# Performance work log

Measured on AMD Instinct MI355X. Metric: run time of the kernel, lower is better.

## Reference

```python
import jax, jax.numpy as jnp
import numpy as np

V, E, H = 32000, 128, 128

def setup_inputs() -> dict:
    key = jax.random.key(0)
    ks = jax.random.split(key, 12)
    s = 0.05
    x = jax.random.randint(ks[0], (256, 512), 0, V)
    emb = jax.random.normal(ks[1], (V, E), jnp.float32) * s
    Wi = jax.random.normal(ks[2], (E + H, H), jnp.float32) * s
    bi = jnp.zeros((H,), jnp.float32)
    Wf = jax.random.normal(ks[3], (E + H, H), jnp.float32) * s
    bf = jnp.zeros((H,), jnp.float32)
    Wc = jax.random.normal(ks[4], (E + H, H), jnp.float32) * s
    bc = jnp.zeros((H,), jnp.float32)
    Wo = jax.random.normal(ks[5], (E + H, H), jnp.float32) * s
    bo = jnp.zeros((H,), jnp.float32)
    Wout = jax.random.normal(ks[6], (H, V), jnp.float32) * s
    bout = jnp.zeros((V,), jnp.float32)
    return {"x": x, "emb": emb, "Wi": Wi, "bi": bi, "Wf": Wf, "bf": bf,
            "Wc": Wc, "bc": bc, "Wo": Wo, "bo": bo, "Wout": Wout, "bout": bout}

def reference(x, emb, Wi, bi, Wf, bf, Wc, bc, Wo, bo, Wout, bout):
    B, T = x.shape
    xe = emb[x]                       # [B, T, E] embedding gather
    xe_t = jnp.swapaxes(xe, 0, 1)     # [T, B, E] for scan over time

    def step(carry, e_t):
        h, c = carry
        comb = jnp.concatenate([e_t, h], axis=1)          # [B, E+H]
        f = jax.nn.sigmoid(comb @ Wf + bf)
        i = jax.nn.sigmoid(comb @ Wi + bi)
        o = jax.nn.sigmoid(comb @ Wo + bo)
        c_ = jnp.tanh(comb @ Wc + bc)
        c = f * c + i * c_
        h = o * jnp.tanh(c)
        return (h, c), None

    h0 = jnp.zeros((B, H), xe.dtype)
    c0 = jnp.zeros((B, H), xe.dtype)
    (h, _), _ = jax.lax.scan(step, (h0, c0), xe_t)
    return h @ Wout + bout            # [B, V] logits from final hidden state
```

## Files before the change

kernel.cpp:

```cpp
#include <hip/hip_runtime.h>

constexpr int TT = 512;
constexpr int BB = 256;
constexpr int HH = 128;
constexpr int VV = 32000;

typedef _Float16 h2 __attribute__((ext_vector_type(2)));
typedef _Float16 f16x4 __attribute__((ext_vector_type(4)));
typedef _Float16 f16x8 __attribute__((ext_vector_type(8)));
typedef float f32x4 __attribute__((ext_vector_type(4)));

struct __align__(16) H2x4 { h2 a, b, c, d; };

__device__ __forceinline__ h2 pkrtz(float a, float b) {
  return __builtin_bit_cast(h2, __builtin_amdgcn_cvt_pkrtz(a, b));
}
__device__ __forceinline__ float fexp2(float x) {
  return __builtin_amdgcn_exp2f(x);
}
__device__ __forceinline__ float frcp(float x) {
  return __builtin_amdgcn_rcpf(x);
}
template <int CTRL>
__device__ __forceinline__ float qmov(float v) {
  return __builtin_bit_cast(
      float, __builtin_amdgcn_mov_dpp(__builtin_bit_cast(int, v), CTRL, 0xf,
                                      0xf, true));
}

constexpr float SC_SIG = -1.4426950408889634f;
constexpr float SC_TANH = 2.8853900817779268f;

__global__ __launch_bounds__(256, 4) void wprep(
    const float* __restrict__ Wi, const float* __restrict__ bi,
    const float* __restrict__ Wf, const float* __restrict__ bf,
    const float* __restrict__ Wc, const float* __restrict__ bc,
    const float* __restrict__ Wo, const float* __restrict__ bo,
    _Float16* __restrict__ Wct, float* __restrict__ bcat) {
  const int n = blockIdx.x;
  const int g = n & 3;
  const int u = n >> 2;
  const float* Wg = (g == 0) ? Wi : (g == 1) ? Wf : (g == 2) ? Wc : Wo;
  const float* bg = (g == 0) ? bi : (g == 1) ? bf : (g == 2) ? bc : bo;
  const float sc = (g == 2) ? SC_TANH : SC_SIG;
  const int k = threadIdx.x;
  Wct[(size_t)n * 256 + k] = (_Float16)(Wg[(size_t)k * HH + u] * sc);
  if (k == 0) bcat[n] = bg[u] * sc;
}

__global__ __launch_bounds__(512, 2) void lstm_rec(
    const int* __restrict__ x, const float* __restrict__ emb,
    const _Float16* __restrict__ Wct, const float* __restrict__ bcat,
    _Float16* __restrict__ hbf) {
  const int b = blockIdx.x;
  const int tid = threadIdx.x;
  const int w = tid >> 6;
  const int l = tid & 63;
  const int n16 = l & 15;
  const int quad = l >> 4;
  const int g = n16 & 3;
  const int nts = n16 >> 2;
  const int u = 16 * w + 4 * nts + quad;
  const int xcol = 4 * u + g;

  __shared__ int xrow[TT];
  __shared__ __align__(16) _Float16 comb[2][HH];
  __shared__ __align__(16) _Float16 xch[64][516];

  xrow[tid] = x[(size_t)b * TT + tid];
  if (tid < HH) comb[0][tid] = (_Float16)0.f;

  f16x8 wh[4][4];
#pragma unroll
  for (int nt = 0; nt < 4; ++nt)
#pragma unroll
    for (int ks = 0; ks < 4; ++ks)
      wh[nt][ks] = *(const f16x8*)(Wct +
                                   (size_t)(64 * w + nt * 16 + n16) * 256 +
                                   128 + ks * 32 + quad * 8);

  f16x8 wfx[4][4];
  f32x4 biasr[4];
#pragma unroll
  for (int nt = 0; nt < 4; ++nt) {
#pragma unroll
    for (int ks = 0; ks < 4; ++ks)
      wfx[nt][ks] = *(const f16x8*)(Wct +
                                    (size_t)(64 * w + nt * 16 + n16) * 256 +
                                    ks * 32 + quad * 8);
    biasr[nt] = *(const f32x4*)(bcat + 64 * w + nt * 16 + quad * 4);
  }

  const float gam = (g == 2) ? -2.f : 1.f;
  const float del = (g == 2) ? 1.f : 0.f;

  const f32x4 ZR4 = {0.f, 0.f, 0.f, 0.f};

  float cst = 0.f;
  float hv = 0.f;
  int buf = 0;

  __syncthreads();

  for (int c = 0; c < 8; ++c) {
#pragma unroll 2
    for (int tt = 0; tt < 4; ++tt) {
      const int vid = xrow[c * 64 + tt * 16 + n16];
      const float* ep = emb + (size_t)vid * HH + quad * 8;
      f16x8 ef[4];
#pragma unroll
      for (int ks = 0; ks < 4; ++ks) {
        const float4 e0 = *(const float4*)(ep + ks * 32);
        const float4 e1 = *(const float4*)(ep + ks * 32 + 4);
        H2x4 q;
        q.a = pkrtz(e0.x, e0.y);
        q.b = pkrtz(e0.z, e0.w);
        q.c = pkrtz(e1.x, e1.y);
        q.d = pkrtz(e1.z, e1.w);
        ef[ks] = __builtin_bit_cast(f16x8, q);
      }
      f32x4 acc[4];
#pragma unroll
      for (int nt = 0; nt < 4; ++nt)
        acc[nt] = __builtin_amdgcn_mfma_f32_16x16x32_f16(wfx[nt][0], ef[0],
                                                         ZR4, 0, 0, 0);
#pragma unroll
      for (int ks = 1; ks < 4; ++ks)
#pragma unroll
        for (int nt = 0; nt < 4; ++nt)
          acc[nt] = __builtin_amdgcn_mfma_f32_16x16x32_f16(wfx[nt][ks], ef[ks],
                                                           acc[nt], 0, 0, 0);
#pragma unroll
      for (int nt = 0; nt < 4; ++nt) {
        const f32x4 av = acc[nt] + biasr[nt];
        _Float16* dst = &xch[tt * 16 + n16][64 * w + nt * 16 + quad * 4];
        *(h2*)dst = pkrtz(av[0], av[1]);
        *(h2*)(dst + 2) = pkrtz(av[2], av[3]);
      }
    }
    __syncthreads();

#pragma unroll 2
    for (int tl = 0; tl < 64; ++tl) {
      const float xe = (float)xch[tl][xcol];

      const _Float16* cb = comb[buf];
      f16x8 hb[4];
#pragma unroll
      for (int ks = 0; ks < 4; ++ks)
        hb[ks] = *(const f16x8*)(cb + ks * 32 + quad * 8);

      f32x4 acc[4];
#pragma unroll
      for (int nt = 0; nt < 4; ++nt)
        acc[nt] = __builtin_amdgcn_mfma_f32_16x16x32_f16(wh[nt][0], hb[0],
                                                         ZR4, 0, 0, 0);
#pragma unroll
      for (int ks = 1; ks < 4; ++ks)
#pragma unroll
        for (int nt = 0; nt < 4; ++nt)
          acc[nt] = __builtin_amdgcn_mfma_f32_16x16x32_f16(wh[nt][ks], hb[ks],
                                                           acc[nt], 0, 0, 0);

      const bool s4 = (n16 & 4) != 0;
      const bool s8 = (n16 & 8) != 0;
      const f32x4 t01 = s4 ? acc[1] : acc[0];
      const f32x4 t23 = s4 ? acc[3] : acc[2];
      const f32x4 avq = s8 ? t23 : t01;
      const bool s1 = (n16 & 1) != 0;
      const bool s2 = (n16 & 2) != 0;
      const float r01 = s1 ? avq[1] : avq[0];
      const float r23 = s1 ? avq[3] : avq[2];
      const float a = (s2 ? r23 : r01) + xe;

      const float act = gam * frcp(1.f + fexp2(a)) + del;

      const float x1 = qmov<0xB1>(act);
      const float x2 = qmov<0x4E>(act);
      const float x3 = qmov<0x4E>(x1);

      cst = x1 * cst + act * x2;
      const float th = 1.f - 2.f * frcp(1.f + fexp2(cst * SC_TANH));
      hv = x3 * th;

      if (g == 0) comb[buf ^ 1][u] = (_Float16)hv;
      __syncthreads();
      buf ^= 1;
    }
  }
  if (g == 0) hbf[(size_t)b * HH + u] = (_Float16)hv;
}

__global__ __launch_bounds__(256, 4) void wout_tr(const float* __restrict__ Wout,
                                                  _Float16* __restrict__ Wt) {
  const int v = blockIdx.x * 256 + threadIdx.x;
#pragma unroll 1
  for (int kc = 0; kc < 16; ++kc) {
    float f[8];
#pragma unroll
    for (int i = 0; i < 8; ++i) f[i] = Wout[(size_t)(kc * 8 + i) * VV + v];
    H2x4 q;
    q.a = pkrtz(f[0], f[1]);
    q.b = pkrtz(f[2], f[3]);
    q.c = pkrtz(f[4], f[5]);
    q.d = pkrtz(f[6], f[7]);
    *(H2x4*)(Wt + (size_t)v * HH + kc * 8) = q;
  }
}

__global__ __launch_bounds__(256, 4) void lstm_out(
    const _Float16* __restrict__ Wt, const _Float16* __restrict__ hbf,
    const float* __restrict__ bout, float* __restrict__ out) {
  const int tid = threadIdx.x;
  const int wv = tid >> 6;
  const int lane = tid & 63;
  const int vblk = blockIdx.x % 250;
  const int batblk = blockIdx.x / 250;
  const int n16 = lane & 15;
  const int quad = lane >> 4;
  const int vbase = vblk * 128 + wv * 32;
  const int batbase = batblk * 64;

  f32x4 acc[4][2] = {};
#pragma unroll
  for (int ks = 0; ks < 4; ++ks) {
    const int k = ks * 32 + quad * 8;
    f16x8 a[4], bf_[2];
#pragma unroll
    for (int mt = 0; mt < 4; ++mt)
      a[mt] = *(const f16x8*)(hbf + (size_t)(batbase + mt * 16 + n16) * HH + k);
#pragma unroll
    for (int vt = 0; vt < 2; ++vt)
      bf_[vt] = *(const f16x8*)(Wt + (size_t)(vbase + vt * 16 + n16) * HH + k);
#pragma unroll
    for (int mt = 0; mt < 4; ++mt)
#pragma unroll
      for (int vt = 0; vt < 2; ++vt)
        acc[mt][vt] = __builtin_amdgcn_mfma_f32_16x16x32_f16(a[mt], bf_[vt],
                                                             acc[mt][vt], 0, 0, 0);
  }
#pragma unroll
  for (int vt = 0; vt < 2; ++vt) {
    const int v = vbase + vt * 16 + n16;
    const float bv = bout[v];
#pragma unroll
    for (int mt = 0; mt < 4; ++mt) {
#pragma unroll
      for (int r = 0; r < 4; ++r) {
        const int bat = batbase + mt * 16 + quad * 4 + r;
        out[(size_t)bat * VV + v] = acc[mt][vt][r] + bv;
      }
    }
  }
}

extern "C" void kernel_launch(void* const* d_in, const int* in_sizes, int n_in,
                              void* d_out, int out_size, void* d_ws,
                              size_t ws_size, hipStream_t stream) {
  const int* x = (const int*)d_in[0];
  const float* emb = (const float*)d_in[1];
  const float* Wi = (const float*)d_in[2];
  const float* bi = (const float*)d_in[3];
  const float* Wf = (const float*)d_in[4];
  const float* bf = (const float*)d_in[5];
  const float* Wc = (const float*)d_in[6];
  const float* bc = (const float*)d_in[7];
  const float* Wo = (const float*)d_in[8];
  const float* bo = (const float*)d_in[9];
  const float* Wout = (const float*)d_in[10];
  const float* bout = (const float*)d_in[11];
  float* out = (float*)d_out;

  _Float16* Wt = (_Float16*)d_ws;
  _Float16* hbf = Wt + (size_t)VV * HH;
  _Float16* Wct = hbf + (size_t)BB * HH;
  float* bcat = (float*)(Wct + 512 * 256);

  wprep<<<512, 256, 0, stream>>>(Wi, bi, Wf, bf, Wc, bc, Wo, bo, Wct, bcat);
  wout_tr<<<VV / 256, 256, 0, stream>>>(Wout, Wt);
  lstm_rec<<<BB, 512, 0, stream>>>(x, emb, Wct, bcat, hbf);
  lstm_out<<<(VV / 128) * (BB / 64), 256, 0, stream>>>(Wt, hbf, bout, out);
}
```

Measured before the change: 411.5 us.

## Replace per-step MFMA recurrent matvec with per-thread fdot2 dot products

The recurrent h·W_h product in each time step moves off the MFMA units. Each thread now holds one full 128-wide weight row in registers as packed half2 and computes its gate pre-activation with 64 v_dot2 instructions over broadcast LDS reads of h. This drops the lane-select shuffle of MFMA outputs and the cost of pushing an N=1 matvec through MFMA, which wastes most of its columns. The trade is roughly 64 dot2 ops plus 16 broadcast LDS loads per thread per step, and higher VGPR use, which may hurt occupancy.

```diff
diff --git a/kernel.cpp b/kernel.cpp
--- a/kernel.cpp
+++ b/kernel.cpp
@@ -20,6 +20,9 @@
 }
 __device__ __forceinline__ float frcp(float x) {
   return __builtin_amdgcn_rcpf(x);
+}
+__device__ __forceinline__ float fdot2(h2 a, h2 b, float c) {
+  return __builtin_amdgcn_fdot2(a, b, c, false);
 }
 template <int CTRL>
 __device__ __forceinline__ float qmov(float v) {
@@ -54,14 +57,12 @@
     _Float16* __restrict__ hbf) {
   const int b = blockIdx.x;
   const int tid = threadIdx.x;
+  const int g = tid & 3;
+  const int u = tid >> 2;
   const int w = tid >> 6;
   const int l = tid & 63;
   const int n16 = l & 15;
   const int quad = l >> 4;
-  const int g = n16 & 3;
-  const int nts = n16 >> 2;
-  const int u = 16 * w + 4 * nts + quad;
-  const int xcol = 4 * u + g;
 
   __shared__ int xrow[TT];
   __shared__ __align__(16) _Float16 comb[2][HH];
@@ -70,14 +71,18 @@
   xrow[tid] = x[(size_t)b * TT + tid];
   if (tid < HH) comb[0][tid] = (_Float16)0.f;
 
-  f16x8 wh[4][4];
-#pragma unroll
-  for (int nt = 0; nt < 4; ++nt)
-#pragma unroll
-    for (int ks = 0; ks < 4; ++ks)
-      wh[nt][ks] = *(const f16x8*)(Wct +
-                                   (size_t)(64 * w + nt * 16 + n16) * 256 +
-                                   128 + ks * 32 + quad * 8);
+  h2 wh2[64];
+  {
+    const _Float16* wp = Wct + (size_t)tid * 256 + 128;
+#pragma unroll
+    for (int j = 0; j < 16; ++j) {
+      const H2x4 q = __builtin_bit_cast(H2x4, *(const f16x8*)(wp + 8 * j));
+      wh2[4 * j + 0] = q.a;
+      wh2[4 * j + 1] = q.b;
+      wh2[4 * j + 2] = q.c;
+      wh2[4 * j + 3] = q.d;
+    }
+  }
 
   f16x8 wfx[4][4];
   f32x4 biasr[4];
@@ -142,36 +147,19 @@
 
 #pragma unroll 2
     for (int tl = 0; tl < 64; ++tl) {
-      const float xe = (float)xch[tl][xcol];
+      const float xe = (float)xch[tl][tid];
 
       const _Float16* cb = comb[buf];
-      f16x8 hb[4];
-#pragma unroll
-      for (int ks = 0; ks < 4; ++ks)
-        hb[ks] = *(const f16x8*)(cb + ks * 32 + quad * 8);
-
-      f32x4 acc[4];
-#pragma unroll
-      for (int nt = 0; nt < 4; ++nt)
-        acc[nt] = __builtin_amdgcn_mfma_f32_16x16x32_f16(wh[nt][0], hb[0],
-                                                         ZR4, 0, 0, 0);
-#pragma unroll
-      for (int ks = 1; ks < 4; ++ks)
-#pragma unroll
-        for (int nt = 0; nt < 4; ++nt)
-          acc[nt] = __builtin_amdgcn_mfma_f32_16x16x32_f16(wh[nt][ks], hb[ks],
-                                                           acc[nt], 0, 0, 0);
-
-      const bool s4 = (n16 & 4) != 0;
-      const bool s8 = (n16 & 8) != 0;
-      const f32x4 t01 = s4 ? acc[1] : acc[0];
-      const f32x4 t23 = s4 ? acc[3] : acc[2];
-      const f32x4 avq = s8 ? t23 : t01;
-      const bool s1 = (n16 & 1) != 0;
-      const bool s2 = (n16 & 2) != 0;
-      const float r01 = s1 ? avq[1] : avq[0];
-      const float r23 = s1 ? avq[3] : avq[2];
-      const float a = (s2 ? r23 : r01) + xe;
+      float s0 = 0.f, s1 = 0.f, s2 = 0.f, s3 = 0.f;
+#pragma unroll
+      for (int j = 0; j < 16; ++j) {
+        const H2x4 hq = __builtin_bit_cast(H2x4, *(const f16x8*)(cb + 8 * j));
+        s0 = fdot2(hq.a, wh2[4 * j + 0], s0);
+        s1 = fdot2(hq.b, wh2[4 * j + 1], s1);
+        s2 = fdot2(hq.c, wh2[4 * j + 2], s2);
+        s3 = fdot2(hq.d, wh2[4 * j + 3], s3);
+      }
+      const float a = (s0 + s1) + (s2 + s3) + xe;
 
       const float act = gam * frcp(1.f + fexp2(a)) + del;
 
```

New measurement: 439.7 us. 1.07x slower.

## Split recurrent LSTM across 16 waves per batch row and merge prep kernels

Applied to the files above, without the earlier changes.

The recurrent kernel now launches 1024 threads per batch element, so each of 16 waves computes two 16-gate tiles instead of four. This halves the serial MFMA chain per timestep, and the input-projection weights are reloaded per chunk instead of being held in registers. The bias now seeds the MFMA accumulator directly, and the two weight-prep kernels are fused into one launch. The trade-off is one block per CU with 16 waves per barrier, which may raise the cost of the per-step __syncthreads, and half the lanes in each wave compute duplicate gate values.

```diff
diff --git a/kernel.cpp b/kernel.cpp
--- a/kernel.cpp
+++ b/kernel.cpp
@@ -31,24 +31,41 @@
 constexpr float SC_SIG = -1.4426950408889634f;
 constexpr float SC_TANH = 2.8853900817779268f;
 
-__global__ __launch_bounds__(256, 4) void wprep(
+__global__ __launch_bounds__(256, 4) void prep(
     const float* __restrict__ Wi, const float* __restrict__ bi,
     const float* __restrict__ Wf, const float* __restrict__ bf,
     const float* __restrict__ Wc, const float* __restrict__ bc,
     const float* __restrict__ Wo, const float* __restrict__ bo,
-    _Float16* __restrict__ Wct, float* __restrict__ bcat) {
-  const int n = blockIdx.x;
-  const int g = n & 3;
-  const int u = n >> 2;
-  const float* Wg = (g == 0) ? Wi : (g == 1) ? Wf : (g == 2) ? Wc : Wo;
-  const float* bg = (g == 0) ? bi : (g == 1) ? bf : (g == 2) ? bc : bo;
-  const float sc = (g == 2) ? SC_TANH : SC_SIG;
-  const int k = threadIdx.x;
-  Wct[(size_t)n * 256 + k] = (_Float16)(Wg[(size_t)k * HH + u] * sc);
-  if (k == 0) bcat[n] = bg[u] * sc;
-}
-
-__global__ __launch_bounds__(512, 2) void lstm_rec(
+    _Float16* __restrict__ Wct, float* __restrict__ bcat,
+    const float* __restrict__ Wout, _Float16* __restrict__ Wt) {
+  if (blockIdx.x < 512) {
+    const int n = blockIdx.x;
+    const int g = n & 3;
+    const int u = n >> 2;
+    const float* Wg = (g == 0) ? Wi : (g == 1) ? Wf : (g == 2) ? Wc : Wo;
+    const float* bg = (g == 0) ? bi : (g == 1) ? bf : (g == 2) ? bc : bo;
+    const float sc = (g == 2) ? SC_TANH : SC_SIG;
+    const int k = threadIdx.x;
+    Wct[(size_t)n * 256 + k] = (_Float16)(Wg[(size_t)k * HH + u] * sc);
+    if (k == 0) bcat[n] = bg[u] * sc;
+  } else {
+    const int v = (blockIdx.x - 512) * 256 + threadIdx.x;
+#pragma unroll 1
+    for (int kc = 0; kc < 16; ++kc) {
+      float f[8];
+#pragma unroll
+      for (int i = 0; i < 8; ++i) f[i] = Wout[(size_t)(kc * 8 + i) * VV + v];
+      H2x4 q;
+      q.a = pkrtz(f[0], f[1]);
+      q.b = pkrtz(f[2], f[3]);
+      q.c = pkrtz(f[4], f[5]);
+      q.d = pkrtz(f[6], f[7]);
+      *(H2x4*)(Wt + (size_t)v * HH + kc * 8) = q;
+    }
+  }
+}
+
+__global__ __launch_bounds__(1024, 1) void lstm_rec(
     const int* __restrict__ x, const float* __restrict__ emb,
     const _Float16* __restrict__ Wct, const float* __restrict__ bcat,
     _Float16* __restrict__ hbf) {
@@ -59,37 +76,25 @@
   const int n16 = l & 15;
   const int quad = l >> 4;
   const int g = n16 & 3;
-  const int nts = n16 >> 2;
-  const int u = 16 * w + 4 * nts + quad;
-  const int xcol = 4 * u + g;
+  const int nt_sel = (n16 >> 2) & 1;
+  const int u = 8 * w + 4 * nt_sel + quad;
+  const int xei = 4 * u + g;
 
   __shared__ int xrow[TT];
   __shared__ __align__(16) _Float16 comb[2][HH];
   __shared__ __align__(16) _Float16 xch[64][516];
 
-  xrow[tid] = x[(size_t)b * TT + tid];
+  if (tid < TT) xrow[tid] = x[(size_t)b * TT + tid];
   if (tid < HH) comb[0][tid] = (_Float16)0.f;
 
-  f16x8 wh[4][4];
-#pragma unroll
-  for (int nt = 0; nt < 4; ++nt)
+  f16x8 wh[2][4];
+#pragma unroll
+  for (int nt = 0; nt < 2; ++nt)
 #pragma unroll
     for (int ks = 0; ks < 4; ++ks)
       wh[nt][ks] = *(const f16x8*)(Wct +
-                                   (size_t)(64 * w + nt * 16 + n16) * 256 +
+                                   (size_t)(32 * w + nt * 16 + n16) * 256 +
                                    128 + ks * 32 + quad * 8);
-
-  f16x8 wfx[4][4];
-  f32x4 biasr[4];
-#pragma unroll
-  for (int nt = 0; nt < 4; ++nt) {
-#pragma unroll
-    for (int ks = 0; ks < 4; ++ks)
-      wfx[nt][ks] = *(const f16x8*)(Wct +
-                                    (size_t)(64 * w + nt * 16 + n16) * 256 +
-                                    ks * 32 + quad * 8);
-    biasr[nt] = *(const f32x4*)(bcat + 64 * w + nt * 16 + quad * 4);
-  }
 
   const float gam = (g == 2) ? -2.f : 1.f;
   const float del = (g == 2) ? 1.f : 0.f;
@@ -103,46 +108,58 @@
   __syncthreads();
 
   for (int c = 0; c < 8; ++c) {
-#pragma unroll 2
-    for (int tt = 0; tt < 4; ++tt) {
-      const int vid = xrow[c * 64 + tt * 16 + n16];
-      const float* ep = emb + (size_t)vid * HH + quad * 8;
-      f16x8 ef[4];
-#pragma unroll
-      for (int ks = 0; ks < 4; ++ks) {
-        const float4 e0 = *(const float4*)(ep + ks * 32);
-        const float4 e1 = *(const float4*)(ep + ks * 32 + 4);
-        H2x4 q;
-        q.a = pkrtz(e0.x, e0.y);
-        q.b = pkrtz(e0.z, e0.w);
-        q.c = pkrtz(e1.x, e1.y);
-        q.d = pkrtz(e1.z, e1.w);
-        ef[ks] = __builtin_bit_cast(f16x8, q);
-      }
-      f32x4 acc[4];
-#pragma unroll
-      for (int nt = 0; nt < 4; ++nt)
-        acc[nt] = __builtin_amdgcn_mfma_f32_16x16x32_f16(wfx[nt][0], ef[0],
-                                                         ZR4, 0, 0, 0);
-#pragma unroll
-      for (int ks = 1; ks < 4; ++ks)
-#pragma unroll
-        for (int nt = 0; nt < 4; ++nt)
-          acc[nt] = __builtin_amdgcn_mfma_f32_16x16x32_f16(wfx[nt][ks], ef[ks],
-                                                           acc[nt], 0, 0, 0);
-#pragma unroll
-      for (int nt = 0; nt < 4; ++nt) {
-        const f32x4 av = acc[nt] + biasr[nt];
-        _Float16* dst = &xch[tt * 16 + n16][64 * w + nt * 16 + quad * 4];
-        *(h2*)dst = pkrtz(av[0], av[1]);
-        *(h2*)(dst + 2) = pkrtz(av[2], av[3]);
+    {
+      f16x8 wfx[2][4];
+      f32x4 biasr[2];
+#pragma unroll
+      for (int nt = 0; nt < 2; ++nt) {
+#pragma unroll
+        for (int ks = 0; ks < 4; ++ks)
+          wfx[nt][ks] =
+              *(const f16x8*)(Wct + (size_t)(32 * w + nt * 16 + n16) * 256 +
+                              ks * 32 + quad * 8);
+        biasr[nt] = *(const f32x4*)(bcat + 32 * w + nt * 16 + quad * 4);
+      }
+#pragma unroll 1
+      for (int tt = 0; tt < 4; ++tt) {
+        const int vid = xrow[c * 64 + tt * 16 + n16];
+        const float* ep = emb + (size_t)vid * HH + quad * 8;
+        f16x8 ef[4];
+#pragma unroll
+        for (int ks = 0; ks < 4; ++ks) {
+          const float4 e0 = *(const float4*)(ep + ks * 32);
+          const float4 e1 = *(const float4*)(ep + ks * 32 + 4);
+          H2x4 q;
+          q.a = pkrtz(e0.x, e0.y);
+          q.b = pkrtz(e0.z, e0.w);
+          q.c = pkrtz(e1.x, e1.y);
+          q.d = pkrtz(e1.z, e1.w);
+          ef[ks] = __builtin_bit_cast(f16x8, q);
+        }
+        f32x4 acc[2];
+#pragma unroll
+        for (int nt = 0; nt < 2; ++nt)
+          acc[nt] = __builtin_amdgcn_mfma_f32_16x16x32_f16(wfx[nt][0], ef[0],
+                                                           biasr[nt], 0, 0, 0);
+#pragma unroll
+        for (int ks = 1; ks < 4; ++ks)
+#pragma unroll
+          for (int nt = 0; nt < 2; ++nt)
+            acc[nt] = __builtin_amdgcn_mfma_f32_16x16x32_f16(
+                wfx[nt][ks], ef[ks], acc[nt], 0, 0, 0);
+#pragma unroll
+        for (int nt = 0; nt < 2; ++nt) {
+          _Float16* dst = &xch[tt * 16 + n16][32 * w + nt * 16 + quad * 4];
+          *(h2*)dst = pkrtz(acc[nt][0], acc[nt][1]);
+          *(h2*)(dst + 2) = pkrtz(acc[nt][2], acc[nt][3]);
+        }
       }
     }
     __syncthreads();
 
 #pragma unroll 2
     for (int tl = 0; tl < 64; ++tl) {
-      const float xe = (float)xch[tl][xcol];
+      const float xe = (float)xch[tl][xei];
 
       const _Float16* cb = comb[buf];
       f16x8 hb[4];
@@ -150,25 +167,21 @@
       for (int ks = 0; ks < 4; ++ks)
         hb[ks] = *(const f16x8*)(cb + ks * 32 + quad * 8);
 
-      f32x4 acc[4];
-#pragma unroll
-      for (int nt = 0; nt < 4; ++nt)
-        acc[nt] = __builtin_amdgcn_mfma_f32_16x16x32_f16(wh[nt][0], hb[0],
-                                                         ZR4, 0, 0, 0);
-#pragma unroll
-      for (int ks = 1; ks < 4; ++ks)
-#pragma unroll
-        for (int nt = 0; nt < 4; ++nt)
-          acc[nt] = __builtin_amdgcn_mfma_f32_16x16x32_f16(wh[nt][ks], hb[ks],
-                                                           acc[nt], 0, 0, 0);
-
-      const bool s4 = (n16 & 4) != 0;
-      const bool s8 = (n16 & 8) != 0;
-      const f32x4 t01 = s4 ? acc[1] : acc[0];
-      const f32x4 t23 = s4 ? acc[3] : acc[2];
-      const f32x4 avq = s8 ? t23 : t01;
-      const bool s1 = (n16 & 1) != 0;
-      const bool s2 = (n16 & 2) != 0;
+      f32x4 acc0 = __builtin_amdgcn_mfma_f32_16x16x32_f16(wh[0][0], hb[0],
+                                                          ZR4, 0, 0, 0);
+      f32x4 acc1 = __builtin_amdgcn_mfma_f32_16x16x32_f16(wh[1][0], hb[0],
+                                                          ZR4, 0, 0, 0);
+#pragma unroll
+      for (int ks = 1; ks < 4; ++ks) {
+        acc0 = __builtin_amdgcn_mfma_f32_16x16x32_f16(wh[0][ks], hb[ks], acc0,
+                                                      0, 0, 0);
+        acc1 = __builtin_amdgcn_mfma_f32_16x16x32_f16(wh[1][ks], hb[ks], acc1,
+                                                      0, 0, 0);
+      }
+
+      const f32x4 avq = nt_sel ? acc1 : acc0;
+      const bool s1 = (g & 1) != 0;
+      const bool s2 = (g & 2) != 0;
       const float r01 = s1 ? avq[1] : avq[0];
       const float r23 = s1 ? avq[3] : avq[2];
       const float a = (s2 ? r23 : r01) + xe;
@@ -183,29 +196,12 @@
       const float th = 1.f - 2.f * frcp(1.f + fexp2(cst * SC_TANH));
       hv = x3 * th;
 
-      if (g == 0) comb[buf ^ 1][u] = (_Float16)hv;
+      if (g == 0 && n16 < 8) comb[buf ^ 1][u] = (_Float16)hv;
       __syncthreads();
       buf ^= 1;
     }
   }
-  if (g == 0) hbf[(size_t)b * HH + u] = (_Float16)hv;
-}
-
-__global__ __launch_bounds__(256, 4) void wout_tr(const float* __restrict__ Wout,
-                                                  _Float16* __restrict__ Wt) {
-  const int v = blockIdx.x * 256 + threadIdx.x;
-#pragma unroll 1
-  for (int kc = 0; kc < 16; ++kc) {
-    float f[8];
-#pragma unroll
-    for (int i = 0; i < 8; ++i) f[i] = Wout[(size_t)(kc * 8 + i) * VV + v];
-    H2x4 q;
-    q.a = pkrtz(f[0], f[1]);
-    q.b = pkrtz(f[2], f[3]);
-    q.c = pkrtz(f[4], f[5]);
-    q.d = pkrtz(f[6], f[7]);
-    *(H2x4*)(Wt + (size_t)v * HH + kc * 8) = q;
-  }
+  if (g == 0 && n16 < 8) hbf[(size_t)b * HH + u] = (_Float16)hv;
 }
 
 __global__ __launch_bounds__(256, 4) void lstm_out(
@@ -276,8 +272,8 @@
   _Float16* Wct = hbf + (size_t)BB * HH;
   float* bcat = (float*)(Wct + 512 * 256);
 
-  wprep<<<512, 256, 0, stream>>>(Wi, bi, Wf, bf, Wc, bc, Wo, bo, Wct, bcat);
-  wout_tr<<<VV / 256, 256, 0, stream>>>(Wout, Wt);
-  lstm_rec<<<BB, 512, 0, stream>>>(x, emb, Wct, bcat, hbf);
+  prep<<<512 + VV / 256, 256, 0, stream>>>(Wi, bi, Wf, bf, Wc, bc, Wo, bo,
+                                           Wct, bcat, Wout, Wt);
+  lstm_rec<<<BB, 1024, 0, stream>>>(x, emb, Wct, bcat, hbf);
   lstm_out<<<(VV / 128) * (BB / 64), 256, 0, stream>>>(Wt, hbf, bout, out);
 }
```

Result: slower. 495.1 us (+20.3%).
